# Kernel optimization log

Hardware: AMD Instinct MI355X
Metric: run time of the kernel (lower is better)

## Reference

```python
import jax, jax.numpy as jnp
import numpy as np

D_MODEL = 1024
N_HEADS = 16
D_K = D_MODEL // N_HEADS
B, S = 2, 2048


def setup_inputs() -> dict:
    key = jax.random.key(0)
    ks = jax.random.split(key, 11)
    def lin(kw, kb, fan_in):
        bound = 1.0 / np.sqrt(fan_in)
        W = jax.random.uniform(kw, (fan_in, D_MODEL), jnp.float32, -bound, bound)
        b = jax.random.uniform(kb, (D_MODEL,), jnp.float32, -bound, bound)
        return W, b
    Wq, bq = lin(ks[0], ks[1], D_MODEL)
    Wk, bk = lin(ks[2], ks[3], D_MODEL)
    Wv, bv = lin(ks[4], ks[5], D_MODEL)
    Wo, bo = lin(ks[6], ks[7], D_MODEL)
    q = jax.random.normal(ks[8], (B, S, D_MODEL), jnp.float32)
    k = jax.random.normal(ks[9], (B, S, D_MODEL), jnp.float32)
    v = jax.random.normal(ks[10], (B, S, D_MODEL), jnp.float32)
    return {"q": q, "k": k, "v": v,
            "Wq": Wq, "bq": bq, "Wk": Wk, "bk": bk,
            "Wv": Wv, "bv": bv, "Wo": Wo, "bo": bo}


def reference(q, k, v, Wq, bq, Wk, bk, Wv, bv, Wo, bo):
    Bz, Sq, _ = q.shape
    def split_heads(x):  # [B,S,D] -> [B,H,S,d_k]
        return x.reshape(x.shape[0], x.shape[1], N_HEADS, D_K).transpose(0, 2, 1, 3)
    qh = split_heads(q @ Wq + bq)
    kh = split_heads(k @ Wk + bk)
    vh = split_heads(v @ Wv + bv)
    scores = jnp.einsum("bhqd,bhkd->bhqk", qh, kh) / jnp.sqrt(jnp.float32(D_K))
    attn = jax.nn.softmax(scores, axis=-1)
    out = jnp.einsum("bhqk,bhkd->bhqd", attn, vh)
    out = out.transpose(0, 2, 1, 3).reshape(Bz, Sq, D_MODEL)
    return out @ Wo + bo
```

## Files before the change

### kernel.cpp

```cpp
#include <hip/hip_runtime.h>
#include <hip/hip_bf16.h>
#include <stdint.h>

typedef __bf16 bf16;
typedef __bf16 bf16x8 __attribute__((ext_vector_type(8)));
typedef __bf16 bf16x4 __attribute__((ext_vector_type(4)));
typedef float  f32x4  __attribute__((ext_vector_type(4)));
typedef float  f32x16 __attribute__((ext_vector_type(16)));
typedef uint32_t u32;

#define MFMA16(a,b,c) __builtin_amdgcn_mfma_f32_16x16x32_bf16((a),(b),(c),0,0,0)
#define MFMA32(a,b,c) __builtin_amdgcn_mfma_f32_32x32x16_bf16((a),(b),(c),0,0,0)

#define QSCL 0.1803368801111204f

__device__ __forceinline__ u32 sx32(u32 x) {
    return (u32)__shfl_xor((int)x, 32, 64);
}
__device__ __forceinline__ float swapred_max(float v) {
    return fmaxf(v, __builtin_bit_cast(float, sx32(__builtin_bit_cast(u32, v))));
}
__device__ __forceinline__ float swapred_sum(float v) {
    return v + __builtin_bit_cast(float, sx32(__builtin_bit_cast(u32, v)));
}
__device__ __forceinline__ u32 pkbf(float lo, float hi) {
    union { bf16 h[2]; u32 u; } un;
    un.h[0] = (bf16)lo; un.h[1] = (bf16)hi;
    return un.u;
}
__device__ __forceinline__ void pack_frags(const float* p, int hi, bf16x8& f0, bf16x8& f1) {
    u32 k01 = pkbf(p[0],  p[1]),  k23 = pkbf(p[2],  p[3]);
    u32 k45 = pkbf(p[4],  p[5]),  k67 = pkbf(p[6],  p[7]);
    u32 k89 = pkbf(p[8],  p[9]),  kab = pkbf(p[10], p[11]);
    u32 kcd = pkbf(p[12], p[13]), kef = pkbf(p[14], p[15]);
    u32 x01 = sx32(k01), x23 = sx32(k23), x45 = sx32(k45), x67 = sx32(k67);
    u32 x89 = sx32(k89), xab = sx32(kab), xcd = sx32(kcd), xef = sx32(kef);
    union { u32 w[4]; bf16x8 v; } u0, u1;
    u0.w[0] = hi ? x45 : k01;  u0.w[1] = hi ? x67 : k23;
    u0.w[2] = hi ? k45 : x01;  u0.w[3] = hi ? k67 : x23;
    u1.w[0] = hi ? xcd : k89;  u1.w[1] = hi ? xef : kab;
    u1.w[2] = hi ? kcd : x89;  u1.w[3] = hi ? kef : xab;
    f0 = u0.v; f1 = u1.v;
}

__device__ __forceinline__ void transpose_body(const float* __restrict__ W, bf16* __restrict__ Wt,
                                               float scale, int n0, int k0) {
    __shared__ bf16 t[64][65];
    for (int i = 0; i < 16; ++i) {
        int idx = threadIdx.x + i * 256, r = idx >> 6, c = idx & 63;
        t[r][c] = (bf16)(W[(size_t)(k0 + r) * 1024 + n0 + c] * scale);
    }
    __syncthreads();
    for (int i = 0; i < 16; ++i) {
        int idx = threadIdx.x + i * 256, r = idx >> 6, c = idx & 63;
        Wt[(size_t)(n0 + r) * 1024 + k0 + c] = t[c][r];
    }
}
__global__ __launch_bounds__(256) void k_transpose_w(const float* __restrict__ W,
                                                     bf16* __restrict__ Wt, float scale) {
    transpose_body(W, Wt, scale, blockIdx.x * 64, blockIdx.y * 64);
}
__global__ __launch_bounds__(256) void k_transpose_w4(const float* __restrict__ Wq, const float* __restrict__ Wk,
                                                      const float* __restrict__ Wv, const float* __restrict__ Wo,
                                                      bf16* __restrict__ Wtq, bf16* __restrict__ Wtk,
                                                      bf16* __restrict__ Wtv, bf16* __restrict__ Wto) {
    int z = blockIdx.z;
    const float* W = (z == 0) ? Wq : (z == 1) ? Wk : (z == 2) ? Wv : Wo;
    bf16* Wt = (z == 0) ? Wtq : (z == 1) ? Wtk : (z == 2) ? Wtv : Wto;
    transpose_body(W, Wt, (z == 0) ? QSCL : 1.0f, blockIdx.x * 64, blockIdx.y * 64);
}

template <int A_F32, int B_F32>
__device__ __forceinline__ void gemm_tile2(const void* __restrict__ Ap, const void* __restrict__ Btp,
                                           const float* __restrict__ bias, float bscale,
                                           void* __restrict__ Cp, int out_mode, int m0, int n0,
                                           bf16 (*As)[64], bf16 (*Bs)[64]) {
    const int tid = threadIdx.x;
    const int wid = tid >> 6, lane = tid & 63, lg = lane >> 4, lm = lane & 15;
    const int wr = wid >> 1, wc = wid & 1;
    const int grow = tid >> 3, gcol = (tid & 7) << 3;

    f32x4 acc[4][4] = {};

    for (int kt = 0; kt < 16; ++kt) {
        const int k0 = kt << 6;
        __syncthreads();
#pragma unroll
        for (int p = 0; p < 4; ++p) {
            const int r = p * 32 + grow;
            if constexpr (A_F32) {
                const float* A = (const float*)Ap;
                const float* src = A + (size_t)(m0 + r) * 1024 + k0 + gcol;
                float4 v0 = *(const float4*)src;
                float4 v1 = *(const float4*)(src + 4);
                bf16x8 w = {(bf16)v0.x, (bf16)v0.y, (bf16)v0.z, (bf16)v0.w,
                            (bf16)v1.x, (bf16)v1.y, (bf16)v1.z, (bf16)v1.w};
                *(bf16x8*)&As[r][gcol] = w;
            } else {
                const bf16* A = (const bf16*)Ap;
                __builtin_amdgcn_global_load_lds(
                    (const __attribute__((address_space(1))) void*)(A + (size_t)(m0 + r) * 1024 + k0 + gcol),
                    (__attribute__((address_space(3))) void*)(&As[p * 32 + wid * 8][0]), 16, 0, 0);
            }
            if constexpr (B_F32) {
                const float* B = (const float*)Btp;
                const float* src = B + (size_t)(n0 + r) * 1024 + k0 + gcol;
                float4 v0 = *(const float4*)src;
                float4 v1 = *(const float4*)(src + 4);
                bf16x8 w = {(bf16)v0.x, (bf16)v0.y, (bf16)v0.z, (bf16)v0.w,
                            (bf16)v1.x, (bf16)v1.y, (bf16)v1.z, (bf16)v1.w};
                *(bf16x8*)&Bs[r][gcol] = w;
            } else {
                const bf16* Bt = (const bf16*)Btp;
                __builtin_amdgcn_global_load_lds(
                    (const __attribute__((address_space(1))) void*)(Bt + (size_t)(n0 + r) * 1024 + k0 + gcol),
                    (__attribute__((address_space(3))) void*)(&Bs[p * 32 + wid * 8][0]), 16, 0, 0);
            }
        }
        __syncthreads();
#pragma unroll
        for (int kk = 0; kk < 2; ++kk) {
            bf16x8 a[4], b[4];
#pragma unroll
            for (int i = 0; i < 4; ++i) a[i] = *(const bf16x8*)&As[wr * 64 + i * 16 + lm][kk * 32 + lg * 8];
#pragma unroll
            for (int j = 0; j < 4; ++j) b[j] = *(const bf16x8*)&Bs[wc * 64 + j * 16 + lm][kk * 32 + lg * 8];
#pragma unroll
            for (int i = 0; i < 4; ++i)
#pragma unroll
                for (int j = 0; j < 4; ++j) acc[i][j] = MFMA16(a[i], b[j], acc[i][j]);
        }
    }

    for (int i = 0; i < 4; ++i) {
        for (int j = 0; j < 4; ++j) {
            int col = n0 + wc * 64 + j * 16 + lm;
            for (int q = 0; q < 4; ++q) {
                int row = m0 + wr * 64 + i * 16 + lg * 4 + q;
                if (out_mode == 0) {
                    float val = acc[i][j][q] + bscale * bias[col];
                    int bb = row >> 11, s = row & 2047, h = col >> 6, d = col & 63;
                    ((bf16*)Cp)[(((size_t)bb * 16 + h) * 2048 + s) * 64 + d] = (bf16)val;
                } else {
                    float val = acc[i][j][q] + bias[row];
                    size_t idx = (((size_t)(col >> 11) * 16 + (row >> 6)) * 64 + (row & 63)) * 2048 + (col & 2047);
                    ((bf16*)Cp)[idx] = (bf16)val;
                }
            }
        }
    }
}

__device__ __forceinline__ void tile_decode(int r, int& m0, int& n0) {
    int xcd = r & 7, slot = (r >> 3) & 3, n = (r >> 5) & 7;
    m0 = (xcd * 4 + slot) * 128;
    n0 = n * 128;
}
__device__ __forceinline__ void tile_decode_vt(int r, int& m0, int& n0) {
    int xcd = r & 7, loc = r >> 3;
    int nslot = loc & 3, m = loc >> 2;
    n0 = (xcd * 4 + nslot) * 128;
    m0 = m * 128;
}

__global__ __launch_bounds__(256, 4) void k_gemm_proj(const float* __restrict__ A,
                                                      const bf16* __restrict__ Bt,
                                                      const float* __restrict__ bias, float bscale,
                                                      void* __restrict__ Cp) {
    __shared__ bf16 As[128][64];
    __shared__ bf16 Bs[128][64];
    int m0, n0;
    tile_decode(blockIdx.x, m0, n0);
    gemm_tile2<1, 0>((const void*)A, (const void*)Bt, bias, bscale, Cp, 0, m0, n0, As, Bs);
}

__global__ __launch_bounds__(256, 4) void k_gemm_vt(const bf16* __restrict__ Wtv,
                                                    const float* __restrict__ v,
                                                    const float* __restrict__ bias,
                                                    bf16* __restrict__ Vtb) {
    __shared__ bf16 As[128][64];
    __shared__ bf16 Bs[128][64];
    int m0, n0;
    tile_decode_vt(blockIdx.x, m0, n0);
    gemm_tile2<0, 1>((const void*)Wtv, (const void*)v, bias, 1.0f, (void*)Vtb, 2, m0, n0, As, Bs);
}

__global__ __launch_bounds__(256, 4) void k_gemm_qkv(const float* __restrict__ q, const float* __restrict__ k,
                                                     const float* __restrict__ v,
                                                     const bf16* __restrict__ Wtq, const bf16* __restrict__ Wtk,
                                                     const bf16* __restrict__ Wtv,
                                                     const float* __restrict__ bq, const float* __restrict__ bk,
                                                     const float* __restrict__ bv,
                                                     bf16* __restrict__ Qb, bf16* __restrict__ Kb,
                                                     bf16* __restrict__ Vtb) {
    __shared__ bf16 As[128][64];
    __shared__ bf16 Bs[128][64];
    int l = blockIdx.x, z = l >> 8, r = l & 255;
    int m0, n0;
    if (z == 2) {
        tile_decode_vt(r, m0, n0);
        gemm_tile2<0, 1>((const void*)Wtv, (const void*)v, bv, 1.0f, (void*)Vtb, 2, m0, n0, As, Bs);
    } else {
        tile_decode(r, m0, n0);
        const float* A  = (z == 0) ? q : k;
        const bf16* Bt  = (z == 0) ? Wtq : Wtk;
        const float* bias = (z == 0) ? bq : bk;
        float bscale = (z == 0) ? QSCL : 1.0f;
        bf16* Cp = (z == 0) ? Qb : Kb;
        gemm_tile2<1, 0>((const void*)A, (const void*)Bt, bias, bscale, (void*)Cp, 0, m0, n0, As, Bs);
    }
}

__global__ __launch_bounds__(256, 4) void k_gemm_out(const bf16* __restrict__ A,
                                                     const bf16* __restrict__ Bt,
                                                     const float* __restrict__ bias,
                                                     float* __restrict__ C) {
    __shared__ bf16 As[128][64];
    __shared__ bf16 Bs[64][64];
    const int tid = threadIdx.x;
    const int wid = tid >> 6, lane = tid & 63, lg = lane >> 4, lm = lane & 15;
    const int grow = tid >> 3, gcol = (tid & 7) << 3;
    const int r = blockIdx.x;
    const int xcd = r & 7, loc = r >> 3;
    const int mslot = loc & 3, n = loc >> 2;
    const int m0 = (xcd * 4 + mslot) * 128, n0 = n * 64;

    f32x4 acc[2][4] = {};

    for (int kt = 0; kt < 16; ++kt) {
        const int k0 = kt << 6;
        __syncthreads();
#pragma unroll
        for (int p = 0; p < 4; ++p)
            __builtin_amdgcn_global_load_lds(
                (const __attribute__((address_space(1))) void*)(A + (size_t)(m0 + p * 32 + grow) * 1024 + k0 + gcol),
                (__attribute__((address_space(3))) void*)(&As[p * 32 + wid * 8][0]), 16, 0, 0);
#pragma unroll
        for (int p = 0; p < 2; ++p)
            __builtin_amdgcn_global_load_lds(
                (const __attribute__((address_space(1))) void*)(Bt + (size_t)(n0 + p * 32 + grow) * 1024 + k0 + gcol),
                (__attribute__((address_space(3))) void*)(&Bs[p * 32 + wid * 8][0]), 16, 0, 0);
        __syncthreads();
#pragma unroll
        for (int kk = 0; kk < 2; ++kk) {
            bf16x8 a[2], b[4];
#pragma unroll
            for (int i = 0; i < 2; ++i) a[i] = *(const bf16x8*)&As[wid * 32 + i * 16 + lm][kk * 32 + lg * 8];
#pragma unroll
            for (int j = 0; j < 4; ++j) b[j] = *(const bf16x8*)&Bs[j * 16 + lm][kk * 32 + lg * 8];
#pragma unroll
            for (int i = 0; i < 2; ++i)
#pragma unroll
                for (int j = 0; j < 4; ++j) acc[i][j] = MFMA16(a[i], b[j], acc[i][j]);
        }
    }

    for (int i = 0; i < 2; ++i) {
        for (int j = 0; j < 4; ++j) {
            int col = n0 + j * 16 + lm;
            float bv = bias[col];
            for (int q = 0; q < 4; ++q) {
                int row = m0 + wid * 32 + i * 16 + lg * 4 + q;
                C[(size_t)row * 1024 + col] = acc[i][j][q] + bv;
            }
        }
    }
}

__global__ __launch_bounds__(512, 2) void k_attn(const bf16* __restrict__ Q,
                                                 const bf16* __restrict__ Kb,
                                                 const bf16* __restrict__ Vt,
                                                 bf16* __restrict__ Out) {
    __shared__ bf16 Ks[2][64 * 64];
    __shared__ bf16 Vs[2][64 * 64];
    const int tid = threadIdx.x;
    const int wid = tid >> 6, lane = tid & 63;
    const int lm = lane & 31, hi = lane >> 5;
    const int bid = blockIdx.x;
    const int bh = bid & 31, qt = bid >> 5;
    const int bb = bh >> 4, h = bh & 15;
    const int qrow = qt * 256 + wid * 32 + lm;
    const size_t qk_base = (size_t)bh * (2048 * 64);
    const size_t vt_base = (size_t)bh * (64 * 2048);

    const int srow = tid >> 3, sc8 = tid & 7;
    const int cse = (sc8 ^ (srow & 7)) * 8;
    const bf16* kstage = Kb + qk_base + (size_t)srow * 64 + cse;
    const bf16* vstage = Vt + vt_base + (size_t)srow * 2048 + cse;
    const int ldsoff = wid * 1024;

    bf16x8 qf[4];
    {
        const bf16* qp = Q + qk_base + (size_t)qrow * 64 + hi * 8;
#pragma unroll
        for (int f = 0; f < 4; ++f) qf[f] = *(const bf16x8*)(qp + f * 16);
    }

    f32x16 O0 = {}, O1 = {};
    float mrow = -1e30f, lsum = 0.f;

    const int swz = (lm & 7);

    __builtin_amdgcn_global_load_lds(
        (const __attribute__((address_space(1))) void*)(kstage),
        (__attribute__((address_space(3))) void*)((char*)&Ks[0][0] + ldsoff), 16, 0, 0);
    __builtin_amdgcn_global_load_lds(
        (const __attribute__((address_space(1))) void*)(vstage),
        (__attribute__((address_space(3))) void*)((char*)&Vs[0][0] + ldsoff), 16, 0, 0);
    __syncthreads();

    int cur = 0;
#pragma unroll 1
    for (int kt = 0; kt < 32; ++kt) {
        if (kt + 1 < 32) {
            __builtin_amdgcn_global_load_lds(
                (const __attribute__((address_space(1))) void*)(kstage + (size_t)(kt + 1) * 4096),
                (__attribute__((address_space(3))) void*)((char*)&Ks[cur ^ 1][0] + ldsoff), 16, 0, 0);
            __builtin_amdgcn_global_load_lds(
                (const __attribute__((address_space(1))) void*)(vstage + (size_t)(kt + 1) * 64),
                (__attribute__((address_space(3))) void*)((char*)&Vs[cur ^ 1][0] + ldsoff), 16, 0, 0);
        }

        const char* Ksc = (const char*)&Ks[cur][0];
        const char* Vsc = (const char*)&Vs[cur][0];

        bf16x8 kf0[4], kf1[4];
#pragma unroll
        for (int f = 0; f < 4; ++f) {
            int ch = (f << 1) | hi;
            kf0[f] = *(const bf16x8*)(Ksc + lm * 128 + ((ch ^ swz) << 4));
            kf1[f] = *(const bf16x8*)(Ksc + (lm + 32) * 128 + ((ch ^ swz) << 4));
        }
        bf16x8 vf0[4], vf1[4];
#pragma unroll
        for (int ks = 0; ks < 4; ++ks) {
            int ch = (ks << 1) | hi;
            vf0[ks] = *(const bf16x8*)(Vsc + lm * 128 + ((ch ^ swz) << 4));
            vf1[ks] = *(const bf16x8*)(Vsc + (lm + 32) * 128 + ((ch ^ swz) << 4));
        }

        f32x16 s0 = {}, s1 = {};
#pragma unroll
        for (int f = 0; f < 4; ++f) {
            s0 = MFMA32(kf0[f], qf[f], s0);
            s1 = MFMA32(kf1[f], qf[f], s1);
        }

        float pe0[16], pe1[16];
#pragma unroll
        for (int r = 0; r < 16; ++r) pe0[r] = __builtin_amdgcn_exp2f(s0[r] - mrow);
#pragma unroll
        for (int r = 0; r < 16; ++r) pe1[r] = __builtin_amdgcn_exp2f(s1[r] - mrow);

        float t8[8];
#pragma unroll
        for (int r = 0; r < 8; ++r)
            t8[r] = fmaxf(fmaxf(s0[r], s0[r + 8]), fmaxf(s1[r], s1[r + 8]));
#pragma unroll
        for (int st = 4; st; st >>= 1)
#pragma unroll
            for (int r = 0; r < st; ++r) t8[r] = fmaxf(t8[r], t8[r + st]);
        float pm = swapred_max(t8[0]);

        if (!__all(pm <= mrow + 8.0f)) {
            float mnew = fmaxf(mrow, pm);
            float corr = __builtin_amdgcn_exp2f(mrow - mnew);
            lsum *= corr;
            O0 *= corr;
            O1 *= corr;
            mrow = mnew;
#pragma unroll
            for (int r = 0; r < 16; ++r) pe0[r] = __builtin_amdgcn_exp2f(s0[r] - mrow);
#pragma unroll
            for (int r = 0; r < 16; ++r) pe1[r] = __builtin_amdgcn_exp2f(s1[r] - mrow);
        }

        float u8[8];
#pragma unroll
        for (int r = 0; r < 8; ++r) u8[r] = (pe0[r] + pe0[r + 8]) + (pe1[r] + pe1[r + 8]);
#pragma unroll
        for (int st = 4; st; st >>= 1)
#pragma unroll
            for (int r = 0; r < st; ++r) u8[r] = u8[r] + u8[r + st];
        lsum += u8[0];

        bf16x8 pf[4];
        pack_frags(pe0, hi, pf[0], pf[1]);
        pack_frags(pe1, hi, pf[2], pf[3]);

#pragma unroll
        for (int ks = 0; ks < 4; ++ks) {
            O0 = MFMA32(vf0[ks], pf[ks], O0);
            O1 = MFMA32(vf1[ks], pf[ks], O1);
        }

        __syncthreads();
        cur ^= 1;
    }

    float lrow = swapred_sum(lsum);
    float inv = 1.0f / lrow;
    bf16* op = Out + ((size_t)bb * 2048 + qrow) * 1024 + h * 64 + 4 * hi;
#pragma unroll
    for (int t = 0; t < 4; ++t) {
        bf16x4 w0, w1;
#pragma unroll
        for (int e = 0; e < 4; ++e) {
            w0[e] = (bf16)(O0[4 * t + e] * inv);
            w1[e] = (bf16)(O1[4 * t + e] * inv);
        }
        *(bf16x4*)(op + 8 * t)      = w0;
        *(bf16x4*)(op + 32 + 8 * t) = w1;
    }
}

extern "C" void kernel_launch(void* const* d_in, const int* in_sizes, int n_in,
                              void* d_out, int out_size, void* d_ws, size_t ws_size,
                              hipStream_t stream) {
    const float* q  = (const float*)d_in[0];
    const float* k  = (const float*)d_in[1];
    const float* v  = (const float*)d_in[2];
    const float* Wq = (const float*)d_in[3];
    const float* bq = (const float*)d_in[4];
    const float* Wk = (const float*)d_in[5];
    const float* bk = (const float*)d_in[6];
    const float* Wv = (const float*)d_in[7];
    const float* bv = (const float*)d_in[8];
    const float* Wo = (const float*)d_in[9];
    const float* bo = (const float*)d_in[10];

    char* ws = (char*)d_ws;
    const size_t MB = 1ull << 20;
    const dim3 twg(16, 16), blk(256);

    if (ws_size >= 40 * MB) {
        bf16* Wtq = (bf16*)(ws + 0 * MB);
        bf16* Wtk = (bf16*)(ws + 2 * MB);
        bf16* Wtv = (bf16*)(ws + 4 * MB);
        bf16* Wto = (bf16*)(ws + 6 * MB);
        bf16* Qb  = (bf16*)(ws + 8 * MB);
        bf16* Kb  = (bf16*)(ws + 16 * MB);
        bf16* Vtb = (bf16*)(ws + 24 * MB);
        bf16* AOb = (bf16*)(ws + 32 * MB);

        k_transpose_w4<<<dim3(16, 16, 4), blk, 0, stream>>>(Wq, Wk, Wv, Wo, Wtq, Wtk, Wtv, Wto);
        k_gemm_qkv<<<768, blk, 0, stream>>>(q, k, v, Wtq, Wtk, Wtv, bq, bk, bv, Qb, Kb, Vtb);
        k_attn<<<256, 512, 0, stream>>>(Qb, Kb, Vtb, AOb);
        k_gemm_out<<<512, blk, 0, stream>>>(AOb, Wto, bo, (float*)d_out);
    } else {
        bf16* Wt   = (bf16*)(ws + 0 * MB);
        bf16* Qb   = (bf16*)(ws + 2 * MB);
        bf16* Kb   = (bf16*)(ws + 10 * MB);
        bf16* Vtb  = (bf16*)(ws + 18 * MB);
        bf16* AOb  = (bf16*)(ws + 26 * MB);

        k_transpose_w<<<twg, blk, 0, stream>>>(Wq, Wt, QSCL);
        k_gemm_proj<<<256, blk, 0, stream>>>(q, Wt, bq, QSCL, (void*)Qb);
        k_transpose_w<<<twg, blk, 0, stream>>>(Wk, Wt, 1.0f);
        k_gemm_proj<<<256, blk, 0, stream>>>(k, Wt, bk, 1.0f, (void*)Kb);
        k_transpose_w<<<twg, blk, 0, stream>>>(Wv, Wt, 1.0f);
        k_gemm_vt<<<256, blk, 0, stream>>>(Wt, v, bv, Vtb);
        k_transpose_w<<<twg, blk, 0, stream>>>(Wo, Wt, 1.0f);
        k_attn<<<256, 512, 0, stream>>>(Qb, Kb, Vtb, AOb);
        k_gemm_out<<<512, blk, 0, stream>>>(AOb, Wt, bo, (float*)d_out);
    }
}
```

Measured before the change: 136.8 us.

## Double-buffer QKV projection GEMM with register prefetch of fp32 tiles

Replaces the single-buffered projection GEMM tile loop with a two-stage pipeline. The next k-tile's fp32 operand is loaded into registers and the bf16 operand is staged to LDS asynchronously while MFMAs run on the current buffer, and there is one barrier per iteration instead of two. The goal is to hide global load latency behind compute. LDS use doubles and launch bounds drop from 4 to 2 blocks per CU, so occupancy falls and register pressure rises.

```diff
diff --git a/kernel.cpp b/kernel.cpp
--- a/kernel.cpp
+++ b/kernel.cpp
@@ -70,66 +70,82 @@
     transpose_body(W, Wt, (z == 0) ? QSCL : 1.0f, blockIdx.x * 64, blockIdx.y * 64);
 }
 
-template <int A_F32, int B_F32>
-__device__ __forceinline__ void gemm_tile2(const void* __restrict__ Ap, const void* __restrict__ Btp,
-                                           const float* __restrict__ bias, float bscale,
-                                           void* __restrict__ Cp, int out_mode, int m0, int n0,
-                                           bf16 (*As)[64], bf16 (*Bs)[64]) {
+template <int F32_IS_A>
+__device__ __forceinline__ void gemm_pipe(const float* __restrict__ P32, const bf16* __restrict__ P16,
+                                          const float* __restrict__ bias, float bscale,
+                                          void* __restrict__ Cp, int out_mode, int m0, int n0,
+                                          bf16 (*S32)[64], bf16 (*L16)[64]) {
     const int tid = threadIdx.x;
     const int wid = tid >> 6, lane = tid & 63, lg = lane >> 4, lm = lane & 15;
     const int wr = wid >> 1, wc = wid & 1;
     const int grow = tid >> 3, gcol = (tid & 7) << 3;
+    const int r32base = F32_IS_A ? m0 : n0;
+    const int r16base = F32_IS_A ? n0 : m0;
 
     f32x4 acc[4][4] = {};
-
+    float4 rA[4][2];
+
+    auto issue32 = [&](int kt) {
+#pragma unroll
+        for (int p = 0; p < 4; ++p) {
+            const float* src = P32 + (size_t)(r32base + p * 32 + grow) * 1024 + (kt << 6) + gcol;
+            rA[p][0] = *(const float4*)src;
+            rA[p][1] = *(const float4*)(src + 4);
+        }
+    };
+    auto write32 = [&](int buf) {
+#pragma unroll
+        for (int p = 0; p < 4; ++p) {
+            bf16x8 w = {(bf16)rA[p][0].x, (bf16)rA[p][0].y, (bf16)rA[p][0].z, (bf16)rA[p][0].w,
+                        (bf16)rA[p][1].x, (bf16)rA[p][1].y, (bf16)rA[p][1].z, (bf16)rA[p][1].w};
+            *(bf16x8*)&S32[buf * 128 + p * 32 + grow][gcol] = w;
+        }
+    };
+    auto stage16 = [&](int kt, int buf) {
+#pragma unroll
+        for (int p = 0; p < 4; ++p)
+            __builtin_amdgcn_global_load_lds(
+                (const __attribute__((address_space(1))) void*)(P16 + (size_t)(r16base + p * 32 + grow) * 1024 + (kt << 6) + gcol),
+                (__attribute__((address_space(3))) void*)(&L16[buf * 128 + p * 32 + wid * 8][0]), 16, 0, 0);
+    };
+
+    issue32(0);
+    stage16(0, 0);
+    write32(0);
+    __syncthreads();
+
+    int buf = 0;
+#pragma unroll 1
     for (int kt = 0; kt < 16; ++kt) {
-        const int k0 = kt << 6;
-        __syncthreads();
-#pragma unroll
-        for (int p = 0; p < 4; ++p) {
-            const int r = p * 32 + grow;
-            if constexpr (A_F32) {
-                const float* A = (const float*)Ap;
-                const float* src = A + (size_t)(m0 + r) * 1024 + k0 + gcol;
-                float4 v0 = *(const float4*)src;
-                float4 v1 = *(const float4*)(src + 4);
-                bf16x8 w = {(bf16)v0.x, (bf16)v0.y, (bf16)v0.z, (bf16)v0.w,
-                            (bf16)v1.x, (bf16)v1.y, (bf16)v1.z, (bf16)v1.w};
-                *(bf16x8*)&As[r][gcol] = w;
-            } else {
-                const bf16* A = (const bf16*)Ap;
-                __builtin_amdgcn_global_load_lds(
-                    (const __attribute__((address_space(1))) void*)(A + (size_t)(m0 + r) * 1024 + k0 + gcol),
-                    (__attribute__((address_space(3))) void*)(&As[p * 32 + wid * 8][0]), 16, 0, 0);
-            }
-            if constexpr (B_F32) {
-                const float* B = (const float*)Btp;
-                const float* src = B + (size_t)(n0 + r) * 1024 + k0 + gcol;
-                float4 v0 = *(const float4*)src;
-                float4 v1 = *(const float4*)(src + 4);
-                bf16x8 w = {(bf16)v0.x, (bf16)v0.y, (bf16)v0.z, (bf16)v0.w,
-                            (bf16)v1.x, (bf16)v1.y, (bf16)v1.z, (bf16)v1.w};
-                *(bf16x8*)&Bs[r][gcol] = w;
-            } else {
-                const bf16* Bt = (const bf16*)Btp;
-                __builtin_amdgcn_global_load_lds(
-                    (const __attribute__((address_space(1))) void*)(Bt + (size_t)(n0 + r) * 1024 + k0 + gcol),
-                    (__attribute__((address_space(3))) void*)(&Bs[p * 32 + wid * 8][0]), 16, 0, 0);
-            }
-        }
-        __syncthreads();
+        if (kt < 15) {
+            issue32(kt + 1);
+            stage16(kt + 1, buf ^ 1);
+        }
 #pragma unroll
         for (int kk = 0; kk < 2; ++kk) {
             bf16x8 a[4], b[4];
 #pragma unroll
-            for (int i = 0; i < 4; ++i) a[i] = *(const bf16x8*)&As[wr * 64 + i * 16 + lm][kk * 32 + lg * 8];
-#pragma unroll
-            for (int j = 0; j < 4; ++j) b[j] = *(const bf16x8*)&Bs[wc * 64 + j * 16 + lm][kk * 32 + lg * 8];
+            for (int i = 0; i < 4; ++i) {
+                if constexpr (F32_IS_A)
+                    a[i] = *(const bf16x8*)&S32[buf * 128 + wr * 64 + i * 16 + lm][kk * 32 + lg * 8];
+                else
+                    a[i] = *(const bf16x8*)&L16[buf * 128 + wr * 64 + i * 16 + lm][kk * 32 + lg * 8];
+            }
+#pragma unroll
+            for (int j = 0; j < 4; ++j) {
+                if constexpr (F32_IS_A)
+                    b[j] = *(const bf16x8*)&L16[buf * 128 + wc * 64 + j * 16 + lm][kk * 32 + lg * 8];
+                else
+                    b[j] = *(const bf16x8*)&S32[buf * 128 + wc * 64 + j * 16 + lm][kk * 32 + lg * 8];
+            }
 #pragma unroll
             for (int i = 0; i < 4; ++i)
 #pragma unroll
                 for (int j = 0; j < 4; ++j) acc[i][j] = MFMA16(a[i], b[j], acc[i][j]);
         }
+        if (kt < 15) write32(buf ^ 1);
+        __syncthreads();
+        buf ^= 1;
     }
 
     for (int i = 0; i < 4; ++i) {
@@ -163,29 +179,29 @@
     m0 = m * 128;
 }
 
-__global__ __launch_bounds__(256, 4) void k_gemm_proj(const float* __restrict__ A,
+__global__ __launch_bounds__(256, 2) void k_gemm_proj(const float* __restrict__ A,
                                                       const bf16* __restrict__ Bt,
                                                       const float* __restrict__ bias, float bscale,
                                                       void* __restrict__ Cp) {
-    __shared__ bf16 As[128][64];
-    __shared__ bf16 Bs[128][64];
+    __shared__ bf16 S32[256][64];
+    __shared__ bf16 L16[256][64];
     int m0, n0;
     tile_decode(blockIdx.x, m0, n0);
-    gemm_tile2<1, 0>((const void*)A, (const void*)Bt, bias, bscale, Cp, 0, m0, n0, As, Bs);
-}
-
-__global__ __launch_bounds__(256, 4) void k_gemm_vt(const bf16* __restrict__ Wtv,
+    gemm_pipe<1>(A, Bt, bias, bscale, Cp, 0, m0, n0, S32, L16);
+}
+
+__global__ __launch_bounds__(256, 2) void k_gemm_vt(const bf16* __restrict__ Wtv,
                                                     const float* __restrict__ v,
                                                     const float* __restrict__ bias,
                                                     bf16* __restrict__ Vtb) {
-    __shared__ bf16 As[128][64];
-    __shared__ bf16 Bs[128][64];
+    __shared__ bf16 S32[256][64];
+    __shared__ bf16 L16[256][64];
     int m0, n0;
     tile_decode_vt(blockIdx.x, m0, n0);
-    gemm_tile2<0, 1>((const void*)Wtv, (const void*)v, bias, 1.0f, (void*)Vtb, 2, m0, n0, As, Bs);
-}
-
-__global__ __launch_bounds__(256, 4) void k_gemm_qkv(const float* __restrict__ q, const float* __restrict__ k,
+    gemm_pipe<0>(v, Wtv, bias, 1.0f, (void*)Vtb, 2, m0, n0, S32, L16);
+}
+
+__global__ __launch_bounds__(256, 2) void k_gemm_qkv(const float* __restrict__ q, const float* __restrict__ k,
                                                      const float* __restrict__ v,
                                                      const bf16* __restrict__ Wtq, const bf16* __restrict__ Wtk,
                                                      const bf16* __restrict__ Wtv,
@@ -193,13 +209,13 @@
                                                      const float* __restrict__ bv,
                                                      bf16* __restrict__ Qb, bf16* __restrict__ Kb,
                                                      bf16* __restrict__ Vtb) {
-    __shared__ bf16 As[128][64];
-    __shared__ bf16 Bs[128][64];
+    __shared__ bf16 S32[256][64];
+    __shared__ bf16 L16[256][64];
     int l = blockIdx.x, z = l >> 8, r = l & 255;
     int m0, n0;
     if (z == 2) {
         tile_decode_vt(r, m0, n0);
-        gemm_tile2<0, 1>((const void*)Wtv, (const void*)v, bv, 1.0f, (void*)Vtb, 2, m0, n0, As, Bs);
+        gemm_pipe<0>(v, Wtv, bv, 1.0f, (void*)Vtb, 2, m0, n0, S32, L16);
     } else {
         tile_decode(r, m0, n0);
         const float* A  = (z == 0) ? q : k;
@@ -207,7 +223,7 @@
         const float* bias = (z == 0) ? bq : bk;
         float bscale = (z == 0) ? QSCL : 1.0f;
         bf16* Cp = (z == 0) ? Qb : Kb;
-        gemm_tile2<1, 0>((const void*)A, (const void*)Bt, bias, bscale, (void*)Cp, 0, m0, n0, As, Bs);
+        gemm_pipe<1>(A, Bt, bias, bscale, (void*)Cp, 0, m0, n0, S32, L16);
     }
 }
 
```

Measured after the change: 146.8 us. 7.3% more time.
